# Performance work log

Hardware: AMD Instinct MI355X
Metric: run time of the kernel (lower is better)

The kernel has to match this reference:

```python
import jax, jax.numpy as jnp
import numpy as np

B, N, C, H = 8, 4096, 512, 8
DH = C // H
EPS = 1e-12  # torch F.normalize eps


def setup_inputs() -> dict:
    key = jax.random.key(0)
    ks = jax.random.split(key, 5)
    x = jax.random.normal(ks[0], (B, N, C), dtype=jnp.float32)
    y = jax.random.normal(ks[1], (B, N, 256), dtype=jnp.float32)
    kv_w = jax.random.normal(ks[2], (2 * C, C), dtype=jnp.float32) / np.sqrt(C)
    q_w = jax.random.normal(ks[3], (C, 256), dtype=jnp.float32) / np.sqrt(256)
    proj_w = jax.random.normal(ks[4], (C, C), dtype=jnp.float32) / np.sqrt(C)
    proj_b = jnp.zeros((C,), dtype=jnp.float32)
    temperature = jnp.ones((H, 1, 1), dtype=jnp.float32)
    return {"x": x, "y": y, "kv_w": kv_w, "q_w": q_w,
            "proj_w": proj_w, "proj_b": proj_b, "temperature": temperature}


def _l2norm(t):
    # torch F.normalize(dim=-1): t / max(||t||, eps)
    n = jnp.sqrt(jnp.sum(t * t, axis=-1, keepdims=True))
    return t / jnp.maximum(n, EPS)


def reference(x, y, kv_w, q_w, proj_w, proj_b, temperature):
    b, n, c = x.shape
    dh = c // H
    kv = (x @ kv_w.T).reshape(b, n, 2, H, dh)
    k = kv[:, :, 0].transpose(0, 2, 3, 1)  # [B,H,dh,N]
    v = kv[:, :, 1].transpose(0, 2, 3, 1)  # [B,H,dh,N]
    q = (y @ q_w.T).reshape(b, n, H, dh).transpose(0, 2, 3, 1)  # [B,H,dh,N]
    q = _l2norm(q)
    k = _l2norm(k)
    attn = jnp.einsum('bhdn,bhen->bhde', q, k) * temperature  # [B,H,dh,dh]
    attn = jax.nn.softmax(attn, axis=-1)
    out = jnp.einsum('bhde,bhen->bhdn', attn, v)  # [B,H,dh,N]
    out = out.transpose(0, 3, 1, 2).reshape(b, n, c)  # [B,N,C]
    return out @ proj_w.T + proj_b
```

## Files before the change

### kernel.cpp

```cpp
#include <hip/hip_runtime.h>
#include <stdint.h>

typedef unsigned short u16;
typedef unsigned int u32;
typedef __attribute__((ext_vector_type(8))) short bf16x8;
typedef __attribute__((ext_vector_type(4))) float f32x4;

typedef __attribute__((address_space(1))) const u32* gas_p;
typedef __attribute__((address_space(3))) u32* las_p;

__device__ __forceinline__ float bf2f(u16 u) {
    union { u32 u; float f; } v; v.u = ((u32)u) << 16; return v.f;
}
__device__ __forceinline__ u16 f2bf(float f) {
    union { __bf16 b; u16 u; } v; v.b = (__bf16)f; return v.u;
}
__device__ __forceinline__ uint4 cvt8(float4 a, float4 b) {
    union { u16 h[8]; uint4 v; } o;
    o.h[0] = f2bf(a.x); o.h[1] = f2bf(a.y); o.h[2] = f2bf(a.z); o.h[3] = f2bf(a.w);
    o.h[4] = f2bf(b.x); o.h[5] = f2bf(b.y); o.h[6] = f2bf(b.z); o.h[7] = f2bf(b.w);
    return o.v;
}
__device__ __forceinline__ void gl_lds16(const u16* g, u16* l) {
    __builtin_amdgcn_global_load_lds((gas_p)g, (las_p)l, 16, 0, 0);
}
__device__ __forceinline__ bool is_f32(const void* tp) {
    return *(const u32*)tp == 0x3F800000u;
}

__launch_bounds__(256)
__global__ void convert_inputs(const void* __restrict__ kvwi, const void* __restrict__ qwi,
                               const void* __restrict__ pwi, const void* __restrict__ pbi,
                               const void* __restrict__ tpi,
                               u16* __restrict__ kvwb, u16* __restrict__ qwb,
                               u16* __restrict__ pwb, u16* __restrict__ pbb,
                               float* __restrict__ tempf)
{
    const bool f32m = is_f32(tpi);
    long c = (long)blockIdx.x * 256 + threadIdx.x;
    const void* src; u16* dst; long local;
    if      (c < 65536)  { src = kvwi; dst = kvwb; local = c; }
    else if (c < 81920)  { src = qwi;  dst = qwb;  local = c - 65536; }
    else if (c < 114688) { src = pwi;  dst = pwb;  local = c - 81920; }
    else if (c < 114752) { src = pbi;  dst = pbb;  local = c - 114688; }
    else if (c == 114752) {
        for (int i = 0; i < 8; i++)
            tempf[i] = f32m ? ((const float*)tpi)[i] : bf2f(((const u16*)tpi)[i]);
        return;
    } else return;

    long e0 = local * 8;
    if (f32m) {
        const float* s = (const float*)src + e0;
        *(uint4*)(dst + e0) = cvt8(*(const float4*)s, *(const float4*)(s + 4));
    } else {
        *(uint4*)(dst + e0) = *(const uint4*)((const u16*)src + e0);
    }
}

__launch_bounds__(256)
__global__ void gemm_qkT(const void* __restrict__ xv, const void* __restrict__ yv,
                         const u16* __restrict__ kvwb, const u16* __restrict__ qwb,
                         u16* __restrict__ qT, u16* __restrict__ kT,
                         const void* __restrict__ tp)
{
    __shared__ __align__(16) u16 smem[17408];
    u16 (*As)[32] = (u16(*)[32])smem;
    u16 (*Bs)[32] = (u16(*)[32])(smem + 4096);

    const int z = blockIdx.z;
    const void* Av = z ? xv : yv;
    const u16* Bw  = z ? kvwb : qwb;
    u16* T         = z ? kT : qT;
    const int K    = z ? 512 : 256;

    const bool f32m = is_f32(tp);
    const int t  = threadIdx.x;
    const int n0 = blockIdx.x * 128;
    const int m0 = blockIdx.y * 128;
    const int w = t >> 6, lane = t & 63, quad = lane >> 4, l16 = lane & 15;
    const int wm = (w >> 1) * 64, wn = (w & 1) * 64;

    f32x4 acc[4][4];
#pragma unroll
    for (int i = 0; i < 4; i++)
#pragma unroll
        for (int j = 0; j < 4; j++) acc[i][j] = (f32x4){0.f, 0.f, 0.f, 0.f};

    const int srow = t >> 2, scol = (t & 3) * 8;

    for (int k0 = 0; k0 < K; k0 += 32) {
        if (f32m) {
            const float* Af = (const float*)Av;
#pragma unroll
            for (int p = 0; p < 2; p++) {
                int row = srow + p * 64;
                const float* s = &Af[(long)(m0 + row) * K + k0 + scol];
                *(uint4*)&As[row][scol] = cvt8(*(const float4*)s, *(const float4*)(s + 4));
            }
        } else {
            const u16* Ab = (const u16*)Av;
#pragma unroll
            for (int p = 0; p < 2; p++) {
                int row = srow + p * 64;
                gl_lds16(&Ab[(long)(m0 + row) * K + k0 + scol], &As[row][scol]);
            }
        }
#pragma unroll
        for (int p = 0; p < 2; p++) {
            int row = srow + p * 64;
            gl_lds16(&Bw[(long)(n0 + row) * K + k0 + scol], &Bs[row][scol]);
        }
        __syncthreads();
        bf16x8 af[4], bfr[4];
#pragma unroll
        for (int i = 0; i < 4; i++) af[i]  = *(const bf16x8*)&As[wm + i * 16 + l16][quad * 8];
#pragma unroll
        for (int j = 0; j < 4; j++) bfr[j] = *(const bf16x8*)&Bs[wn + j * 16 + l16][quad * 8];
#pragma unroll
        for (int i = 0; i < 4; i++)
#pragma unroll
            for (int j = 0; j < 4; j++)
                acc[i][j] = __builtin_amdgcn_mfma_f32_16x16x32_bf16(af[i], bfr[j], acc[i][j], 0, 0, 0);
        __syncthreads();
    }

    u16 (*Cs)[136] = (u16(*)[136])smem;
#pragma unroll
    for (int i = 0; i < 4; i++)
#pragma unroll
        for (int j = 0; j < 4; j++)
#pragma unroll
            for (int r = 0; r < 4; r++)
                Cs[wn + j * 16 + l16][wm + i * 16 + quad * 4 + r] = f2bf(acc[i][j][r]);
    __syncthreads();
    const int nrow = t >> 1, mh = (t & 1) * 64;
    const int gn = n0 + nrow;
    const int gm = m0 + mh;
    const int bb = gm >> 12, tok = gm & 4095;
    const long tbase = ((long)(bb * 512 + gn)) * 4096 + tok;
#pragma unroll
    for (int v8 = 0; v8 < 8; v8++)
        *(uint4*)&T[tbase + v8 * 8] = *(uint4*)&Cs[nrow][mh + v8 * 8];
}

__launch_bounds__(256)
__global__ void gram_kernel(const u16* __restrict__ qT, const u16* __restrict__ kT,
                            float* __restrict__ pQK, float* __restrict__ pDQ,
                            float* __restrict__ pDK)
{
    const int nc = blockIdx.x, bh = blockIdx.y;
    const int t = threadIdx.x, w = t >> 6, lane = t & 63;
    const int quad = lane >> 4, l16 = lane & 15;

    __shared__ float red[4][64][64];
    __shared__ float dql[4][64];
    __shared__ float dkl[4][64];

    const u16* qb = qT + (long)bh * 64 * 4096;
    const u16* kb = kT + (long)bh * 64 * 4096;

    f32x4 g[4][4], gq[4], gk[4];
#pragma unroll
    for (int i = 0; i < 4; i++) {
        gq[i] = (f32x4){0.f, 0.f, 0.f, 0.f};
        gk[i] = (f32x4){0.f, 0.f, 0.f, 0.f};
#pragma unroll
        for (int j = 0; j < 4; j++) g[i][j] = (f32x4){0.f, 0.f, 0.f, 0.f};
    }

#pragma unroll
    for (int ks = 0; ks < 4; ks++) {
        const int n = nc * 512 + w * 128 + ks * 32 + quad * 8;
        bf16x8 aq[4], bk[4];
#pragma unroll
        for (int i = 0; i < 4; i++) aq[i] = *(const bf16x8*)&qb[(long)(i * 16 + l16) * 4096 + n];
#pragma unroll
        for (int j = 0; j < 4; j++) bk[j] = *(const bf16x8*)&kb[(long)(j * 16 + l16) * 4096 + n];
#pragma unroll
        for (int i = 0; i < 4; i++)
#pragma unroll
            for (int j = 0; j < 4; j++)
                g[i][j] = __builtin_amdgcn_mfma_f32_16x16x32_bf16(aq[i], bk[j], g[i][j], 0, 0, 0);
#pragma unroll
        for (int i = 0; i < 4; i++) {
            gq[i] = __builtin_amdgcn_mfma_f32_16x16x32_bf16(aq[i], aq[i], gq[i], 0, 0, 0);
            gk[i] = __builtin_amdgcn_mfma_f32_16x16x32_bf16(bk[i], bk[i], gk[i], 0, 0, 0);
        }
    }

#pragma unroll
    for (int i = 0; i < 4; i++)
#pragma unroll
        for (int j = 0; j < 4; j++)
#pragma unroll
            for (int r = 0; r < 4; r++)
                red[w][i * 16 + quad * 4 + r][j * 16 + l16] = g[i][j][r];
    if ((l16 >> 2) == quad) {
        const int rr = l16 & 3;
#pragma unroll
        for (int i = 0; i < 4; i++) {
            float dq = 0.f, dk = 0.f;
#pragma unroll
            for (int r = 0; r < 4; r++)
                if (r == rr) { dq = gq[i][r]; dk = gk[i][r]; }
            dql[w][i * 16 + l16] = dq;
            dkl[w][i * 16 + l16] = dk;
        }
    }
    __syncthreads();

    const long obase = (long)(nc * 64 + bh);
    const int e = t & 63, d0 = (t >> 6) * 16;
    float* o = pQK + obase * 4096;
#pragma unroll
    for (int dd = 0; dd < 16; dd++) {
        int d = d0 + dd;
        o[d * 64 + e] = red[0][d][e] + red[1][d][e] + red[2][d][e] + red[3][d][e];
    }
    if (t < 64) {
        pDQ[obase * 64 + t] = dql[0][t] + dql[1][t] + dql[2][t] + dql[3][t];
        pDK[obase * 64 + t] = dkl[0][t] + dkl[1][t] + dkl[2][t] + dkl[3][t];
    }
}

__launch_bounds__(256)
__global__ void attn_kernel(const float* __restrict__ pQK, const float* __restrict__ pDQ,
                            const float* __restrict__ pDK, const float* __restrict__ tempf,
                            u16* __restrict__ attnT)
{
    const int bh = blockIdx.x;
    const int t = threadIdx.x, w = t >> 6, l = t & 63;
    __shared__ float G[64][65];
    __shared__ float rq[64], rk[64];

#pragma unroll
    for (int ii = 0; ii < 16; ii++) {
        int i = w * 16 + ii;
        float s = 0.f;
#pragma unroll
        for (int nc = 0; nc < 8; nc++) s += pQK[((long)(nc * 64 + bh)) * 4096 + i * 64 + l];
        G[i][l] = s;
    }
    if (t < 64) {
        float sq = 0.f, sk = 0.f;
#pragma unroll
        for (int nc = 0; nc < 8; nc++) {
            sq += pDQ[(nc * 64 + bh) * 64 + t];
            sk += pDK[(nc * 64 + bh) * 64 + t];
        }
        rq[t] = 1.f / fmaxf(sqrtf(sq), 1e-12f);
        rk[t] = 1.f / fmaxf(sqrtf(sk), 1e-12f);
    }
    __syncthreads();

    if (t < 64) {
        const float invq = tempf[bh & 7] * rq[t];
        float mx = -1e30f;
        float row[64];
#pragma unroll
        for (int e = 0; e < 64; e++) {
            float s = G[t][e] * invq * rk[e];
            row[e] = s;
            mx = fmaxf(mx, s);
        }
        float sum = 0.f;
#pragma unroll
        for (int e = 0; e < 64; e++) {
            float p = __expf(row[e] - mx);
            row[e] = p;
            sum += p;
        }
        float inv = 1.f / sum;
#pragma unroll
        for (int e = 0; e < 64; e++)
            attnT[((long)bh * 64 + e) * 64 + t] = f2bf(row[e] * inv);
    }
}

__launch_bounds__(256)
__global__ void wcomb_kernel(const u16* __restrict__ attnT, const u16* __restrict__ pwb,
                             u16* __restrict__ Wc)
{
    const int cc = blockIdx.x, bh = blockIdx.y;
    const int b = bh >> 3, h = bh & 7;
    const int t = threadIdx.x, w = t >> 6, lane = t & 63;
    const int quad = lane >> 4, l16 = lane & 15;
    const int cb = cc * 128 + w * 32;

    f32x4 acc[2][4];
#pragma unroll
    for (int i = 0; i < 2; i++)
#pragma unroll
        for (int j = 0; j < 4; j++) acc[i][j] = (f32x4){0.f, 0.f, 0.f, 0.f};

#pragma unroll
    for (int ks = 0; ks < 2; ks++) {
        const int k = ks * 32 + quad * 8;
        bf16x8 af[2], bfr[4];
#pragma unroll
        for (int i = 0; i < 2; i++)
            af[i] = *(const bf16x8*)&pwb[(long)(cb + i * 16 + l16) * 512 + h * 64 + k];
#pragma unroll
        for (int j = 0; j < 4; j++)
            bfr[j] = *(const bf16x8*)&attnT[((long)bh * 64 + j * 16 + l16) * 64 + k];
#pragma unroll
        for (int i = 0; i < 2; i++)
#pragma unroll
            for (int j = 0; j < 4; j++)
                acc[i][j] = __builtin_amdgcn_mfma_f32_16x16x32_bf16(af[i], bfr[j], acc[i][j], 0, 0, 0);
    }

#pragma unroll
    for (int i = 0; i < 2; i++)
#pragma unroll
        for (int j = 0; j < 4; j++)
#pragma unroll
            for (int r = 0; r < 4; r++) {
                int c = cb + i * 16 + quad * 4 + r;
                int e = j * 16 + l16;
                Wc[((long)(b * 512 + c)) * 512 + h * 64 + e] = f2bf(acc[i][j][r]);
            }
}

__launch_bounds__(256)
__global__ void transpose_kv(const u16* __restrict__ in, u16* __restrict__ out)
{
    __shared__ __align__(16) u16 ts[64][72];
    const int bx = blockIdx.x * 64;
    const int by = blockIdx.y * 64;
    const int t = threadIdx.x;
    const int r = t >> 3, c0 = (t & 7) * 8;
#pragma unroll
    for (int p = 0; p < 2; p++)
        *(uint4*)&ts[r + p * 32][c0] = *(const uint4*)&in[(long)(by + r + p * 32) * 512 + bx + c0];
    __syncthreads();
#pragma unroll
    for (int p = 0; p < 2; p++) {
        int rr = r + p * 32;
        union { u16 h[8]; uint4 v; } tmp;
#pragma unroll
        for (int c = 0; c < 8; c++) tmp.h[c] = ts[c0 + c][rr];
        *(uint4*)&out[(long)(bx + rr) * 512 + by + c0] = tmp.v;
    }
}

__launch_bounds__(256)
__global__ void gemm_bt(const u16* __restrict__ A, const u16* __restrict__ B,
                        u16* __restrict__ C,
                        int K, long sA, long sB, long sC)
{
    __shared__ __align__(16) u16 smem[17408];
    u16 (*As)[32] = (u16(*)[32])smem;
    u16 (*Bs)[32] = (u16(*)[32])(smem + 4096);

    const int t  = threadIdx.x;
    const int n0 = blockIdx.x * 128;
    const int m0 = blockIdx.y * 128;
    const int z  = blockIdx.z;
    A += (long)z * sA;
    B += (long)z * sB;
    C += (long)z * sC;

    const int w = t >> 6, lane = t & 63, quad = lane >> 4, l16 = lane & 15;
    const int wm = (w >> 1) * 64, wn = (w & 1) * 64;

    f32x4 acc[4][4];
#pragma unroll
    for (int i = 0; i < 4; i++)
#pragma unroll
        for (int j = 0; j < 4; j++) acc[i][j] = (f32x4){0.f, 0.f, 0.f, 0.f};

    const int srow = t >> 2, scol = (t & 3) * 8;

    for (int k0 = 0; k0 < K; k0 += 32) {
#pragma unroll
        for (int p = 0; p < 2; p++) {
            int row = srow + p * 64;
            gl_lds16(&A[(long)(m0 + row) * K + k0 + scol], &As[row][scol]);
            gl_lds16(&B[(long)(n0 + row) * K + k0 + scol], &Bs[row][scol]);
        }
        __syncthreads();
        bf16x8 af[4], bfr[4];
#pragma unroll
        for (int i = 0; i < 4; i++) af[i]  = *(const bf16x8*)&As[wm + i * 16 + l16][quad * 8];
#pragma unroll
        for (int j = 0; j < 4; j++) bfr[j] = *(const bf16x8*)&Bs[wn + j * 16 + l16][quad * 8];
#pragma unroll
        for (int i = 0; i < 4; i++)
#pragma unroll
            for (int j = 0; j < 4; j++)
                acc[i][j] = __builtin_amdgcn_mfma_f32_16x16x32_bf16(af[i], bfr[j], acc[i][j], 0, 0, 0);
        __syncthreads();
    }

    u16 (*Cs)[136] = (u16(*)[136])smem;
#pragma unroll
    for (int i = 0; i < 4; i++)
#pragma unroll
        for (int j = 0; j < 4; j++) {
            int nn = wn + j * 16 + l16;
#pragma unroll
            for (int r = 0; r < 4; r++)
                Cs[wm + i * 16 + quad * 4 + r][nn] = f2bf(acc[i][j][r]);
        }
    __syncthreads();
    const int row = t >> 1, c0 = (t & 1) * 64;
#pragma unroll
    for (int v8 = 0; v8 < 8; v8++)
        *(uint4*)&C[(long)(m0 + row) * 512 + n0 + c0 + v8 * 8] = *(uint4*)&Cs[row][c0 + v8 * 8];
}

__launch_bounds__(256)
__global__ void gemm_out(const void* __restrict__ Av, const u16* __restrict__ B,
                         void* __restrict__ Cv, const u16* __restrict__ bias,
                         const void* __restrict__ tp)
{
    __shared__ __align__(16) u16 smem[17408];
    u16 (*As)[32] = (u16(*)[32])smem;
    u16 (*Bs)[32] = (u16(*)[32])(smem + 4096);

    const bool f32m = is_f32(tp);
    const int t  = threadIdx.x;
    const int n0 = blockIdx.x * 128;
    const int m0 = blockIdx.y * 128;
    const int z  = blockIdx.z;
    const long aoff = (long)z * 4096 * 512;
    B += (long)z * 512 * 512;

    const int w = t >> 6, lane = t & 63, quad = lane >> 4, l16 = lane & 15;
    const int wm = (w >> 1) * 64, wn = (w & 1) * 64;

    f32x4 acc[4][4];
#pragma unroll
    for (int i = 0; i < 4; i++)
#pragma unroll
        for (int j = 0; j < 4; j++) acc[i][j] = (f32x4){0.f, 0.f, 0.f, 0.f};

    const int srow = t >> 2, scol = (t & 3) * 8;

    for (int k0 = 0; k0 < 512; k0 += 32) {
        if (f32m) {
            const float* Af = (const float*)Av + aoff;
#pragma unroll
            for (int p = 0; p < 2; p++) {
                int row = srow + p * 64;
                const float* s = &Af[(long)(m0 + row) * 512 + k0 + scol];
                *(uint4*)&As[row][scol] = cvt8(*(const float4*)s, *(const float4*)(s + 4));
            }
        } else {
            const u16* Ab = (const u16*)Av + aoff;
#pragma unroll
            for (int p = 0; p < 2; p++) {
                int row = srow + p * 64;
                gl_lds16(&Ab[(long)(m0 + row) * 512 + k0 + scol], &As[row][scol]);
            }
        }
#pragma unroll
        for (int p = 0; p < 2; p++) {
            int row = srow + p * 64;
            gl_lds16(&B[(long)(n0 + row) * 512 + k0 + scol], &Bs[row][scol]);
        }
        __syncthreads();
        bf16x8 af[4], bfr[4];
#pragma unroll
        for (int i = 0; i < 4; i++) af[i]  = *(const bf16x8*)&As[wm + i * 16 + l16][quad * 8];
#pragma unroll
        for (int j = 0; j < 4; j++) bfr[j] = *(const bf16x8*)&Bs[wn + j * 16 + l16][quad * 8];
#pragma unroll
        for (int i = 0; i < 4; i++)
#pragma unroll
            for (int j = 0; j < 4; j++)
                acc[i][j] = __builtin_amdgcn_mfma_f32_16x16x32_bf16(af[i], bfr[j], acc[i][j], 0, 0, 0);
        __syncthreads();
    }

    if (f32m) {
        float (*Cf)[132] = (float(*)[132])smem;
        float* C = (float*)Cv + (long)z * 4096 * 512;
#pragma unroll
        for (int p = 0; p < 2; p++) {
            __syncthreads();
            if ((w >> 1) == p) {
#pragma unroll
                for (int i = 0; i < 4; i++)
#pragma unroll
                    for (int j = 0; j < 4; j++) {
                        int nn = wn + j * 16 + l16;
                        float bv = bf2f(bias[n0 + nn]);
#pragma unroll
                        for (int r = 0; r < 4; r++)
                            Cf[i * 16 + quad * 4 + r][nn] = acc[i][j][r] + bv;
                    }
            }
            __syncthreads();
            int row = t >> 2, cb = (t & 3) * 32;
#pragma unroll
            for (int v4 = 0; v4 < 8; v4++)
                *(float4*)&C[(long)(m0 + p * 64 + row) * 512 + n0 + cb + v4 * 4] =
                    *(float4*)&Cf[row][cb + v4 * 4];
        }
    } else {
        u16 (*Cs)[136] = (u16(*)[136])smem;
        u16* C = (u16*)Cv + (long)z * 4096 * 512;
#pragma unroll
        for (int i = 0; i < 4; i++)
#pragma unroll
            for (int j = 0; j < 4; j++) {
                int nn = wn + j * 16 + l16;
                float bv = bf2f(bias[n0 + nn]);
#pragma unroll
                for (int r = 0; r < 4; r++)
                    Cs[wm + i * 16 + quad * 4 + r][nn] = f2bf(acc[i][j][r] + bv);
            }
        __syncthreads();
        const int row = t >> 1, c0 = (t & 1) * 64;
#pragma unroll
        for (int v8 = 0; v8 < 8; v8++)
            *(uint4*)&C[(long)(m0 + row) * 512 + n0 + c0 + v8 * 8] = *(uint4*)&Cs[row][c0 + v8 * 8];
    }
}

extern "C" void kernel_launch(void* const* d_in, const int* in_sizes, int n_in,
                              void* d_out, int out_size, void* d_ws, size_t ws_size,
                              hipStream_t stream)
{
    const void* x      = d_in[0];
    const void* y      = d_in[1];
    const void* kv_w   = d_in[2];
    const void* q_w    = d_in[3];
    const void* proj_w = d_in[4];
    const void* proj_b = d_in[5];
    const void* temp   = d_in[6];

    char* ws = (char*)d_ws;
    u16*   kvwb  = (u16*)(ws);
    u16*   qwb   = (u16*)(ws + 1048576);
    u16*   pwb   = (u16*)(ws + 1310720);
    u16*   pbb   = (u16*)(ws + 1835008);
    float* tempf = (float*)(ws + 1836032);
    u16*   qT    = (u16*)(ws + 2097152);
    u16*   kT    = (u16*)(ws + 35651584);
    float* pQK   = (float*)(ws + 69206016);
    float* pDQ   = (float*)(ws + 77594624);
    float* pDK   = (float*)(ws + 77725696);
    u16*   attnT = (u16*)(ws + 77856768);
    u16*   Wc    = (u16*)(ws + 78381056);
    u16*   kvvT  = (u16*)(ws + 82575360);
    u16*   Wfin  = (u16*)(ws + 83099648);

    convert_inputs<<<449, 256, 0, stream>>>(kv_w, q_w, proj_w, proj_b, temp,
                                            kvwb, qwb, pwb, pbb, tempf);
    gemm_qkT<<<dim3(4, 256, 2), 256, 0, stream>>>(x, y, kvwb, qwb, qT, kT, temp);
    gram_kernel<<<dim3(8, 64), 256, 0, stream>>>(qT, kT, pQK, pDQ, pDK);
    attn_kernel<<<64, 256, 0, stream>>>(pQK, pDQ, pDK, tempf, attnT);
    wcomb_kernel<<<dim3(4, 64), 256, 0, stream>>>(attnT, pwb, Wc);
    transpose_kv<<<dim3(8, 8), 256, 0, stream>>>(kvwb + 512 * 512, kvvT);
    gemm_bt<<<dim3(4, 4, 8), 256, 0, stream>>>(Wc, kvvT, Wfin,
                                               512, (long)512 * 512, 0, (long)512 * 512);
    gemm_out<<<dim3(4, 32, 8), 256, 0, stream>>>(x, Wfin, d_out, pbb, temp);
}
```

Measured before the change: 333.9 us.

## Double-buffer GEMM LDS tiles, swizzle LDS layout, and remap blocks per XCD

The three MFMA GEMM kernels now use double-buffered LDS tiles, so the next K-slice is loaded (direct-to-LDS for bf16, or via registers then converted for f32) while MFMAs run on the current slice. This removes one barrier per iteration. The LDS column slots are XOR-swizzled to reduce bank conflicts on the fragment reads. The grids are flattened to 1D with block index decoding that groups tiles by XCD (id&7) for better L2 locality. The cost is more LDS use and register pressure from holding the prefetched f32 values.

```diff
diff --git a/kernel.cpp b/kernel.cpp
--- a/kernel.cpp
+++ b/kernel.cpp
@@ -65,10 +65,15 @@
                          const void* __restrict__ tp)
 {
     __shared__ __align__(16) u16 smem[17408];
-    u16 (*As)[32] = (u16(*)[32])smem;
-    u16 (*Bs)[32] = (u16(*)[32])(smem + 4096);
-
-    const int z = blockIdx.z;
+    u16 (*As)[128][32] = (u16(*)[128][32])smem;
+    u16 (*Bs)[128][32] = (u16(*)[128][32])(smem + 8192);
+
+    const int id = blockIdx.x;
+    const int xcd = id & 7, j = id >> 3;
+    const int z = j >> 7, jj = j & 127;
+    const int n0 = (jj & 3) * 128;
+    const int m0 = (xcd * 32 + (jj >> 2)) * 128;
+
     const void* Av = z ? xv : yv;
     const u16* Bw  = z ? kvwb : qwb;
     u16* T         = z ? kT : qT;
@@ -76,8 +81,6 @@
 
     const bool f32m = is_f32(tp);
     const int t  = threadIdx.x;
-    const int n0 = blockIdx.x * 128;
-    const int m0 = blockIdx.y * 128;
     const int w = t >> 6, lane = t & 63, quad = lane >> 4, l16 = lane & 15;
     const int wm = (w >> 1) * 64, wn = (w & 1) * 64;
 
@@ -85,54 +88,77 @@
 #pragma unroll
     for (int i = 0; i < 4; i++)
 #pragma unroll
-        for (int j = 0; j < 4; j++) acc[i][j] = (f32x4){0.f, 0.f, 0.f, 0.f};
-
-    const int srow = t >> 2, scol = (t & 3) * 8;
-
-    for (int k0 = 0; k0 < K; k0 += 32) {
-        if (f32m) {
-            const float* Af = (const float*)Av;
-#pragma unroll
-            for (int p = 0; p < 2; p++) {
-                int row = srow + p * 64;
-                const float* s = &Af[(long)(m0 + row) * K + k0 + scol];
-                *(uint4*)&As[row][scol] = cvt8(*(const float4*)s, *(const float4*)(s + 4));
+        for (int jx = 0; jx < 4; jx++) acc[i][jx] = (f32x4){0.f, 0.f, 0.f, 0.f};
+
+    const int slot = t & 3, srow = t >> 2;
+    const int csw = (slot ^ ((t >> 3) & 3)) * 8;
+    const int dst = slot * 8;
+    const int qsw = (quad ^ ((l16 >> 1) & 3)) * 8;
+
+    const float* Af = (const float*)Av;
+    const u16*   Ab = (const u16*)Av;
+    const long a0r = (long)(m0 + srow) * K + csw;
+    const long a1r = (long)(m0 + srow + 64) * K + csw;
+    const long b0r = (long)(n0 + srow) * K + csw;
+    const long b1r = (long)(n0 + srow + 64) * K + csw;
+
+    if (f32m) {
+        float4 p0 = *(const float4*)&Af[a0r], p1 = *(const float4*)&Af[a0r + 4];
+        float4 p2 = *(const float4*)&Af[a1r], p3 = *(const float4*)&Af[a1r + 4];
+        *(uint4*)&As[0][srow][dst]      = cvt8(p0, p1);
+        *(uint4*)&As[0][srow + 64][dst] = cvt8(p2, p3);
+    } else {
+        gl_lds16(&Ab[a0r], &As[0][srow][dst]);
+        gl_lds16(&Ab[a1r], &As[0][srow + 64][dst]);
+    }
+    gl_lds16(&Bw[b0r], &Bs[0][srow][dst]);
+    gl_lds16(&Bw[b1r], &Bs[0][srow + 64][dst]);
+    __syncthreads();
+
+    const int nk = K >> 5;
+    for (int kk = 0; kk < nk; kk++) {
+        const int cur = kk & 1, nxt = cur ^ 1;
+        const int k1 = (kk + 1) << 5;
+        const bool more = (kk + 1 < nk);
+        float4 la0, la1, lb0, lb1;
+        if (more) {
+            if (f32m) {
+                la0 = *(const float4*)&Af[a0r + k1];
+                la1 = *(const float4*)&Af[a0r + k1 + 4];
+                lb0 = *(const float4*)&Af[a1r + k1];
+                lb1 = *(const float4*)&Af[a1r + k1 + 4];
+            } else {
+                gl_lds16(&Ab[a0r + k1], &As[nxt][srow][dst]);
+                gl_lds16(&Ab[a1r + k1], &As[nxt][srow + 64][dst]);
             }
-        } else {
-            const u16* Ab = (const u16*)Av;
-#pragma unroll
-            for (int p = 0; p < 2; p++) {
-                int row = srow + p * 64;
-                gl_lds16(&Ab[(long)(m0 + row) * K + k0 + scol], &As[row][scol]);
-            }
-        }
-#pragma unroll
-        for (int p = 0; p < 2; p++) {
-            int row = srow + p * 64;
-            gl_lds16(&Bw[(long)(n0 + row) * K + k0 + scol], &Bs[row][scol]);
+            gl_lds16(&Bw[b0r + k1], &Bs[nxt][srow][dst]);
+            gl_lds16(&Bw[b1r + k1], &Bs[nxt][srow + 64][dst]);
+        }
+        bf16x8 af[4], bfv[4];
+#pragma unroll
+        for (int i = 0; i < 4; i++) af[i]  = *(const bf16x8*)&As[cur][wm + i * 16 + l16][qsw];
+#pragma unroll
+        for (int jx = 0; jx < 4; jx++) bfv[jx] = *(const bf16x8*)&Bs[cur][wn + jx * 16 + l16][qsw];
+#pragma unroll
+        for (int i = 0; i < 4; i++)
+#pragma unroll
+            for (int jx = 0; jx < 4; jx++)
+                acc[i][jx] = __builtin_amdgcn_mfma_f32_16x16x32_bf16(af[i], bfv[jx], acc[i][jx], 0, 0, 0);
+        if (more && f32m) {
+            *(uint4*)&As[nxt][srow][dst]      = cvt8(la0, la1);
+            *(uint4*)&As[nxt][srow + 64][dst] = cvt8(lb0, lb1);
         }
         __syncthreads();
-        bf16x8 af[4], bfr[4];
-#pragma unroll
-        for (int i = 0; i < 4; i++) af[i]  = *(const bf16x8*)&As[wm + i * 16 + l16][quad * 8];
-#pragma unroll
-        for (int j = 0; j < 4; j++) bfr[j] = *(const bf16x8*)&Bs[wn + j * 16 + l16][quad * 8];
-#pragma unroll
-        for (int i = 0; i < 4; i++)
-#pragma unroll
-            for (int j = 0; j < 4; j++)
-                acc[i][j] = __builtin_amdgcn_mfma_f32_16x16x32_bf16(af[i], bfr[j], acc[i][j], 0, 0, 0);
-        __syncthreads();
     }
 
     u16 (*Cs)[136] = (u16(*)[136])smem;
 #pragma unroll
     for (int i = 0; i < 4; i++)
 #pragma unroll
-        for (int j = 0; j < 4; j++)
+        for (int jx = 0; jx < 4; jx++)
 #pragma unroll
             for (int r = 0; r < 4; r++)
-                Cs[wn + j * 16 + l16][wm + i * 16 + quad * 4 + r] = f2bf(acc[i][j][r]);
+                Cs[wn + jx * 16 + l16][wm + i * 16 + quad * 4 + r] = f2bf(acc[i][jx][r]);
     __syncthreads();
     const int nrow = t >> 1, mh = (t & 1) * 64;
     const int gn = n0 + nrow;
@@ -351,13 +377,14 @@
                         int K, long sA, long sB, long sC)
 {
     __shared__ __align__(16) u16 smem[17408];
-    u16 (*As)[32] = (u16(*)[32])smem;
-    u16 (*Bs)[32] = (u16(*)[32])(smem + 4096);
-
+    u16 (*As)[128][32] = (u16(*)[128][32])smem;
+    u16 (*Bs)[128][32] = (u16(*)[128][32])(smem + 8192);
+
+    const int id = blockIdx.x;
+    const int z = id & 7, jj = id >> 3;
+    const int n0 = (jj & 3) * 128;
+    const int m0 = (jj >> 2) * 128;
     const int t  = threadIdx.x;
-    const int n0 = blockIdx.x * 128;
-    const int m0 = blockIdx.y * 128;
-    const int z  = blockIdx.z;
     A += (long)z * sA;
     B += (long)z * sB;
     C += (long)z * sC;
@@ -371,21 +398,37 @@
 #pragma unroll
         for (int j = 0; j < 4; j++) acc[i][j] = (f32x4){0.f, 0.f, 0.f, 0.f};
 
-    const int srow = t >> 2, scol = (t & 3) * 8;
-
-    for (int k0 = 0; k0 < K; k0 += 32) {
-#pragma unroll
-        for (int p = 0; p < 2; p++) {
-            int row = srow + p * 64;
-            gl_lds16(&A[(long)(m0 + row) * K + k0 + scol], &As[row][scol]);
-            gl_lds16(&B[(long)(n0 + row) * K + k0 + scol], &Bs[row][scol]);
-        }
-        __syncthreads();
+    const int slot = t & 3, srow = t >> 2;
+    const int csw = (slot ^ ((t >> 3) & 3)) * 8;
+    const int dst = slot * 8;
+    const int qsw = (quad ^ ((l16 >> 1) & 3)) * 8;
+
+    const long a0r = (long)(m0 + srow) * K + csw;
+    const long a1r = (long)(m0 + srow + 64) * K + csw;
+    const long b0r = (long)(n0 + srow) * K + csw;
+    const long b1r = (long)(n0 + srow + 64) * K + csw;
+
+    gl_lds16(&A[a0r], &As[0][srow][dst]);
+    gl_lds16(&A[a1r], &As[0][srow + 64][dst]);
+    gl_lds16(&B[b0r], &Bs[0][srow][dst]);
+    gl_lds16(&B[b1r], &Bs[0][srow + 64][dst]);
+    __syncthreads();
+
+    const int nk = K >> 5;
+    for (int kk = 0; kk < nk; kk++) {
+        const int cur = kk & 1, nxt = cur ^ 1;
+        const int k1 = (kk + 1) << 5;
+        if (kk + 1 < nk) {
+            gl_lds16(&A[a0r + k1], &As[nxt][srow][dst]);
+            gl_lds16(&A[a1r + k1], &As[nxt][srow + 64][dst]);
+            gl_lds16(&B[b0r + k1], &Bs[nxt][srow][dst]);
+            gl_lds16(&B[b1r + k1], &Bs[nxt][srow + 64][dst]);
+        }
         bf16x8 af[4], bfr[4];
 #pragma unroll
-        for (int i = 0; i < 4; i++) af[i]  = *(const bf16x8*)&As[wm + i * 16 + l16][quad * 8];
-#pragma unroll
-        for (int j = 0; j < 4; j++) bfr[j] = *(const bf16x8*)&Bs[wn + j * 16 + l16][quad * 8];
+        for (int i = 0; i < 4; i++) af[i]  = *(const bf16x8*)&As[cur][wm + i * 16 + l16][qsw];
+#pragma unroll
+        for (int j = 0; j < 4; j++) bfr[j] = *(const bf16x8*)&Bs[cur][wn + j * 16 + l16][qsw];
 #pragma unroll
         for (int i = 0; i < 4; i++)
 #pragma unroll
@@ -417,14 +460,15 @@
                          const void* __restrict__ tp)
 {
     __shared__ __align__(16) u16 smem[17408];
-    u16 (*As)[32] = (u16(*)[32])smem;
-    u16 (*Bs)[32] = (u16(*)[32])(smem + 4096);
+    u16 (*As)[128][32] = (u16(*)[128][32])smem;
+    u16 (*Bs)[128][32] = (u16(*)[128][32])(smem + 8192);
 
     const bool f32m = is_f32(tp);
+    const int id = blockIdx.x;
+    const int z = id & 7, jj = id >> 3;
+    const int n0 = (jj & 3) * 128;
+    const int m0 = (jj >> 2) * 128;
     const int t  = threadIdx.x;
-    const int n0 = blockIdx.x * 128;
-    const int m0 = blockIdx.y * 128;
-    const int z  = blockIdx.z;
     const long aoff = (long)z * 4096 * 512;
     B += (long)z * 512 * 512;
 
@@ -437,41 +481,63 @@
 #pragma unroll
         for (int j = 0; j < 4; j++) acc[i][j] = (f32x4){0.f, 0.f, 0.f, 0.f};
 
-    const int srow = t >> 2, scol = (t & 3) * 8;
-
-    for (int k0 = 0; k0 < 512; k0 += 32) {
-        if (f32m) {
-            const float* Af = (const float*)Av + aoff;
-#pragma unroll
-            for (int p = 0; p < 2; p++) {
-                int row = srow + p * 64;
-                const float* s = &Af[(long)(m0 + row) * 512 + k0 + scol];
-                *(uint4*)&As[row][scol] = cvt8(*(const float4*)s, *(const float4*)(s + 4));
+    const int slot = t & 3, srow = t >> 2;
+    const int csw = (slot ^ ((t >> 3) & 3)) * 8;
+    const int dst = slot * 8;
+    const int qsw = (quad ^ ((l16 >> 1) & 3)) * 8;
+
+    const float* Af = (const float*)Av + aoff;
+    const u16*   Ab = (const u16*)Av + aoff;
+    const long a0r = (long)(m0 + srow) * 512 + csw;
+    const long a1r = (long)(m0 + srow + 64) * 512 + csw;
+    const long b0r = (long)(n0 + srow) * 512 + csw;
+    const long b1r = (long)(n0 + srow + 64) * 512 + csw;
+
+    if (f32m) {
+        float4 p0 = *(const float4*)&Af[a0r], p1 = *(const float4*)&Af[a0r + 4];
+        float4 p2 = *(const float4*)&Af[a1r], p3 = *(const float4*)&Af[a1r + 4];
+        *(uint4*)&As[0][srow][dst]      = cvt8(p0, p1);
+        *(uint4*)&As[0][srow + 64][dst] = cvt8(p2, p3);
+    } else {
+        gl_lds16(&Ab[a0r], &As[0][srow][dst]);
+        gl_lds16(&Ab[a1r], &As[0][srow + 64][dst]);
+    }
+    gl_lds16(&B[b0r], &Bs[0][srow][dst]);
+    gl_lds16(&B[b1r], &Bs[0][srow + 64][dst]);
+    __syncthreads();
+
+    for (int kk = 0; kk < 16; kk++) {
+        const int cur = kk & 1, nxt = cur ^ 1;
+        const int k1 = (kk + 1) << 5;
+        const bool more = (kk + 1 < 16);
+        float4 la0, la1, lb0, lb1;
+        if (more) {
+            if (f32m) {
+                la0 = *(const float4*)&Af[a0r + k1];
+                la1 = *(const float4*)&Af[a0r + k1 + 4];
+                lb0 = *(const float4*)&Af[a1r + k1];
+                lb1 = *(const float4*)&Af[a1r + k1 + 4];
+            } else {
+                gl_lds16(&Ab[a0r + k1], &As[nxt][srow][dst]);
+                gl_lds16(&Ab[a1r + k1], &As[nxt][srow + 64][dst]);
             }
-        } else {
-            const u16* Ab = (const u16*)Av + aoff;
-#pragma unroll
-            for (int p = 0; p < 2; p++) {
-                int row = srow + p * 64;
-                gl_lds16(&Ab[(long)(m0 + row) * 512 + k0 + scol], &As[row][scol]);
-            }
-        }
-#pragma unroll
-        for (int p = 0; p < 2; p++) {
-            int row = srow + p * 64;
-            gl_lds16(&B[(long)(n0 + row) * 512 + k0 + scol], &Bs[row][scol]);
-        }
-        __syncthreads();
+            gl_lds16(&B[b0r + k1], &Bs[nxt][srow][dst]);
+            gl_lds16(&B[b1r + k1], &Bs[nxt][srow + 64][dst]);
+        }
         bf16x8 af[4], bfr[4];
 #pragma unroll
-        for (int i = 0; i < 4; i++) af[i]  = *(const bf16x8*)&As[wm + i * 16 + l16][quad * 8];
-#pragma unroll
-        for (int j = 0; j < 4; j++) bfr[j] = *(const bf16x8*)&Bs[wn + j * 16 + l16][quad * 8];
+        for (int i = 0; i < 4; i++) af[i]  = *(const bf16x8*)&As[cur][wm + i * 16 + l16][qsw];
+#pragma unroll
+        for (int j = 0; j < 4; j++) bfr[j] = *(const bf16x8*)&Bs[cur][wn + j * 16 + l16][qsw];
 #pragma unroll
         for (int i = 0; i < 4; i++)
 #pragma unroll
             for (int j = 0; j < 4; j++)
                 acc[i][j] = __builtin_amdgcn_mfma_f32_16x16x32_bf16(af[i], bfr[j], acc[i][j], 0, 0, 0);
+        if (more && f32m) {
+            *(uint4*)&As[nxt][srow][dst]      = cvt8(la0, la1);
+            *(uint4*)&As[nxt][srow + 64][dst] = cvt8(lb0, lb1);
+        }
         __syncthreads();
     }
 
@@ -551,12 +617,12 @@
 
     convert_inputs<<<449, 256, 0, stream>>>(kv_w, q_w, proj_w, proj_b, temp,
                                             kvwb, qwb, pwb, pbb, tempf);
-    gemm_qkT<<<dim3(4, 256, 2), 256, 0, stream>>>(x, y, kvwb, qwb, qT, kT, temp);
+    gemm_qkT<<<2048, 256, 0, stream>>>(x, y, kvwb, qwb, qT, kT, temp);
     gram_kernel<<<dim3(8, 64), 256, 0, stream>>>(qT, kT, pQK, pDQ, pDK);
     attn_kernel<<<64, 256, 0, stream>>>(pQK, pDQ, pDK, tempf, attnT);
     wcomb_kernel<<<dim3(4, 64), 256, 0, stream>>>(attnT, pwb, Wc);
     transpose_kv<<<dim3(8, 8), 256, 0, stream>>>(kvwb + 512 * 512, kvvT);
-    gemm_bt<<<dim3(4, 4, 8), 256, 0, stream>>>(Wc, kvvT, Wfin,
-                                               512, (long)512 * 512, 0, (long)512 * 512);
-    gemm_out<<<dim3(4, 32, 8), 256, 0, stream>>>(x, Wfin, d_out, pbb, temp);
-}
+    gemm_bt<<<128, 256, 0, stream>>>(Wc, kvvT, Wfin,
+                                     512, (long)512 * 512, 0, (long)512 * 512);
+    gemm_out<<<1024, 256, 0, stream>>>(x, Wfin, d_out, pbb, temp);
+}
```

New measurement: 301.7 us. 1.11x faster.
